# Kernel tuning notes

Measured on AMD Instinct MI355X. Metric: run time of the kernel, lower is better.

Reference implementation:

```python
import jax, jax.numpy as jnp
import numpy as np

N_NODES = 50000
N_EDGES = 800000
IN_CH = 256
OUT_CH = 64
HEADS = 4
NEG_SLOPE = 0.2


def setup_inputs() -> dict:
    key = jax.random.key(0)
    k = jax.random.split(key, 7)
    x = jax.random.normal(k[0], (N_NODES, IN_CH), dtype=jnp.float32)
    edge_index = jax.random.randint(k[1], (2, N_EDGES), 0, N_NODES, dtype=jnp.int32)
    # Glorot-style init for the linear projection and attention vectors
    W = jax.random.normal(k[2], (IN_CH, HEADS * OUT_CH), dtype=jnp.float32) / np.sqrt(IN_CH)
    att_src = jax.random.normal(k[3], (HEADS, OUT_CH), dtype=jnp.float32) / np.sqrt(OUT_CH)
    att_dst = jax.random.normal(k[4], (HEADS, OUT_CH), dtype=jnp.float32) / np.sqrt(OUT_CH)
    bias = jnp.zeros((HEADS * OUT_CH,), dtype=jnp.float32)
    return {"x": x, "edge_index": edge_index, "W": W,
            "att_src": att_src, "att_dst": att_dst, "bias": bias}


def reference(x, edge_index, W, att_src, att_dst, bias):
    N = x.shape[0]
    # PyG GATConv default: add self-loops
    loop = jnp.arange(N, dtype=edge_index.dtype)
    src = jnp.concatenate([edge_index[0], loop])
    dst = jnp.concatenate([edge_index[1], loop])

    h = (x @ W).reshape(N, HEADS, OUT_CH)          # [N,H,C]
    a_src = jnp.einsum('nhc,hc->nh', h, att_src)    # [N,H]
    a_dst = jnp.einsum('nhc,hc->nh', h, att_dst)    # [N,H]

    alpha = a_src[src] + a_dst[dst]                 # [E,H]
    alpha = jax.nn.leaky_relu(alpha, NEG_SLOPE)

    # segment softmax over edges grouped by destination node
    amax = jax.ops.segment_max(alpha, dst, num_segments=N)
    amax = jnp.where(jnp.isfinite(amax), amax, 0.0)
    e = jnp.exp(alpha - amax[dst])
    denom = jax.ops.segment_sum(e, dst, num_segments=N)
    coef = e / (denom[dst] + 1e-16)                 # [E,H]

    msg = coef[..., None] * h[src]                  # [E,H,C]
    out = jax.ops.segment_sum(msg, dst, num_segments=N)  # [N,H,C]
    out = out.reshape(N, HEADS * OUT_CH) + bias
    return jax.nn.relu(out)
```

## Files before the change

### kernel.cpp

```cpp
#include <hip/hip_runtime.h>
#include <hip/hip_bf16.h>

#define HC 256
#define NEG_SLOPE 0.2f
#define BM 64
#define BK 64
#define LDK 72

typedef short short8_t __attribute__((ext_vector_type(8)));
typedef float float4_t __attribute__((ext_vector_type(4)));
typedef int   int4_t   __attribute__((ext_vector_type(4)));

__device__ __forceinline__ unsigned short f2bf(float f) {
  unsigned u = __float_as_uint(f);
  return (unsigned short)((u + 0x7fffu + ((u >> 16) & 1u)) >> 16);
}
__device__ __forceinline__ float bf2f(unsigned short b) {
  return __uint_as_float(((unsigned)b) << 16);
}

__global__ void wt_kernel(const float* __restrict__ W, unsigned short* __restrict__ Wt)
{
  const int k = blockIdx.x;
  const int n = threadIdx.x;
  Wt[n * 256 + k] = f2bf(W[k * 256 + n]);
}

__global__ __launch_bounds__(256) void gemm_mfma(
    const float* __restrict__ x, const unsigned short* __restrict__ Wt,
    const float* __restrict__ att_src, const float* __restrict__ att_dst,
    unsigned short* __restrict__ h, float* __restrict__ a_src,
    float* __restrict__ a_dst, int nnodes)
{
  __shared__ unsigned short As[BM * LDK];
  __shared__ unsigned short Bs[256 * LDK];
  const int t    = threadIdx.x;
  const int wv   = t >> 6;
  const int lane = t & 63;
  const int r0   = blockIdx.x * BM;

  float4_t acc[4][4] = {};

  for (int k0 = 0; k0 < 256; k0 += BK) {
    __syncthreads();
    {
      const int row = t >> 2, kc = (t & 3) * 16;
      const int gr = r0 + row;
      float4 xv[4];
      if (gr < nnodes) {
        const float4* p = (const float4*)(x + (size_t)gr * 256 + k0 + kc);
        xv[0] = p[0]; xv[1] = p[1]; xv[2] = p[2]; xv[3] = p[3];
      } else {
        xv[0] = xv[1] = xv[2] = xv[3] = make_float4(0.f, 0.f, 0.f, 0.f);
      }
      const float* f = (const float*)xv;
      unsigned pk[8];
      #pragma unroll
      for (int i = 0; i < 8; ++i) {
        __hip_bfloat162 b2 = __float22bfloat162_rn(make_float2(f[2 * i], f[2 * i + 1]));
        pk[i] = *(unsigned*)&b2;
      }
      uint4* d = (uint4*)&As[row * LDK + kc];
      d[0] = make_uint4(pk[0], pk[1], pk[2], pk[3]);
      d[1] = make_uint4(pk[4], pk[5], pk[6], pk[7]);
    }
    #pragma unroll
    for (int it = 0; it < 4; ++it) {
      const int n = it * 64 + (t >> 2);
      const int kc = (t & 3) * 16;
      const uint4* g = (const uint4*)(Wt + (size_t)n * 256 + k0 + kc);
      uint4 v0 = g[0], v1 = g[1];
      uint4* d = (uint4*)&Bs[n * LDK + kc];
      d[0] = v0; d[1] = v1;
    }
    __syncthreads();

    #pragma unroll
    for (int ks = 0; ks < 2; ++ks) {
      const int ko = ks * 32 + (lane >> 4) * 8;
      short8_t af[4], bfr[4];
      #pragma unroll
      for (int mt = 0; mt < 4; ++mt)
        af[mt] = *(const short8_t*)&As[(16 * mt + (lane & 15)) * LDK + ko];
      #pragma unroll
      for (int nt = 0; nt < 4; ++nt)
        bfr[nt] = *(const short8_t*)&Bs[(64 * wv + 16 * nt + (lane & 15)) * LDK + ko];
      #pragma unroll
      for (int mt = 0; mt < 4; ++mt)
        #pragma unroll
        for (int nt = 0; nt < 4; ++nt)
          acc[mt][nt] = __builtin_amdgcn_mfma_f32_16x16x32_bf16(
              af[mt], bfr[nt], acc[mt][nt], 0, 0, 0);
    }
  }

  const int q = lane >> 4, l15 = lane & 15;
  float atts[4], attd[4];
  #pragma unroll
  for (int nt = 0; nt < 4; ++nt) {
    atts[nt] = att_src[wv * 64 + 16 * nt + l15];
    attd[nt] = att_dst[wv * 64 + 16 * nt + l15];
  }

  #pragma unroll
  for (int mt = 0; mt < 4; ++mt) {
    #pragma unroll
    for (int reg = 0; reg < 4; ++reg) {
      const int row = r0 + 16 * mt + 4 * q + reg;
      const bool ok = row < nnodes;
      float ps = 0.f, pd = 0.f;
      #pragma unroll
      for (int nt = 0; nt < 4; ++nt) {
        const float v = acc[mt][nt][reg];
        if (ok) h[(size_t)row * 256 + 64 * wv + 16 * nt + l15] = f2bf(v);
        ps += v * atts[nt];
        pd += v * attd[nt];
      }
      #pragma unroll
      for (int off = 8; off; off >>= 1) {
        ps += __shfl_down(ps, off, 16);
        pd += __shfl_down(pd, off, 16);
      }
      if (ok && l15 == 0) {
        a_src[row * 4 + wv] = ps;
        a_dst[row * 4 + wv] = pd;
      }
    }
  }
}

__global__ void deg_count(const int* __restrict__ ei, int* __restrict__ deg, int E)
{
  const int e = blockIdx.x * blockDim.x + threadIdx.x;
  if (e >= E) return;
  atomicAdd(&deg[ei[E + e]], 1);
}

__global__ __launch_bounds__(256) void scan_p1(const int* __restrict__ deg,
                                               int* __restrict__ bsum, int n)
{
  __shared__ int ws[4];
  const int t = threadIdx.x, lane = t & 63, wv = t >> 6;
  const int base = blockIdx.x * 1024 + t * 4;
  int4 v = make_int4(0, 0, 0, 0);
  if (base + 3 < n) v = *(const int4*)&deg[base];
  else {
    if (base + 0 < n) v.x = deg[base + 0];
    if (base + 1 < n) v.y = deg[base + 1];
    if (base + 2 < n) v.z = deg[base + 2];
  }
  int s = (v.x + v.y) + (v.z + v.w);
  #pragma unroll
  for (int off = 32; off; off >>= 1) s += __shfl_down(s, off, 64);
  if (lane == 0) ws[wv] = s;
  __syncthreads();
  if (t == 0) bsum[blockIdx.x] = (ws[0] + ws[1]) + (ws[2] + ws[3]);
}

__global__ __launch_bounds__(1024) void scan_p2(const int* __restrict__ bsum,
                                                int* __restrict__ boff,
                                                int* __restrict__ rowptr,
                                                int nb, int n)
{
  __shared__ int wsum[16], woff[16];
  const int t = threadIdx.x, lane = t & 63, wv = t >> 6;
  int v = (t < nb) ? bsum[t] : 0;
  int sc = v;
  #pragma unroll
  for (int off = 1; off < 64; off <<= 1) {
    int u = __shfl_up(sc, off, 64);
    if (lane >= off) sc += u;
  }
  if (lane == 63) wsum[wv] = sc;
  __syncthreads();
  if (t == 0) {
    int run = 0;
    #pragma unroll
    for (int i = 0; i < 16; ++i) { int x = wsum[i]; woff[i] = run; run += x; }
    rowptr[n] = run;
  }
  __syncthreads();
  if (t < nb) boff[t] = woff[wv] + sc - v;
}

__global__ __launch_bounds__(256) void scan_p3(const int* __restrict__ deg,
                                               const int* __restrict__ boff,
                                               int* __restrict__ rowptr,
                                               int* __restrict__ cursor, int n)
{
  __shared__ int wsum[4], woff[4];
  const int t = threadIdx.x, lane = t & 63, wv = t >> 6;
  const int base = blockIdx.x * 1024 + t * 4;
  int4 v = make_int4(0, 0, 0, 0);
  if (base + 3 < n) v = *(const int4*)&deg[base];
  else {
    if (base + 0 < n) v.x = deg[base + 0];
    if (base + 1 < n) v.y = deg[base + 1];
    if (base + 2 < n) v.z = deg[base + 2];
  }
  const int s = (v.x + v.y) + (v.z + v.w);
  int sc = s;
  #pragma unroll
  for (int off = 1; off < 64; off <<= 1) {
    int u = __shfl_up(sc, off, 64);
    if (lane >= off) sc += u;
  }
  if (lane == 63) wsum[wv] = sc;
  __syncthreads();
  if (t == 0) {
    int run = 0;
    #pragma unroll
    for (int i = 0; i < 4; ++i) { int x = wsum[i]; woff[i] = run; run += x; }
  }
  __syncthreads();
  int excl = boff[blockIdx.x] + woff[wv] + (sc - s);
  int4 r;
  r.x = excl;
  r.y = r.x + v.x;
  r.z = r.y + v.y;
  r.w = r.z + v.z;
  if (base + 3 < n) {
    *(int4*)&rowptr[base] = r;
    *(int4*)&cursor[base] = r;
  } else {
    if (base + 0 < n) { rowptr[base + 0] = r.x; cursor[base + 0] = r.x; }
    if (base + 1 < n) { rowptr[base + 1] = r.y; cursor[base + 1] = r.y; }
    if (base + 2 < n) { rowptr[base + 2] = r.z; cursor[base + 2] = r.z; }
  }
}

__global__ __launch_bounds__(256) void fill_csr(
    const int* __restrict__ ei, int* __restrict__ cursor,
    int* __restrict__ csr_src, int E, int nnodes)
{
  const int g    = blockIdx.x & 7;
  const int bg   = blockIdx.x >> 3;
  const int nbg  = gridDim.x >> 3;
  const int gsz  = (nnodes + 7) >> 3;
  const int dlo  = g * gsz;
  const int dhi  = min(dlo + gsz, nnodes);

  for (int e = bg * 256 + threadIdx.x; e < E; e += nbg * 256) {
    const int d = ei[E + e];
    if (d < dlo || d >= dhi) continue;
    const int pos = atomicAdd(&cursor[d], 1);
    csr_src[pos] = ei[e];
  }
}

__device__ __forceinline__ float4 ld_h(const unsigned short* __restrict__ h,
                                       int row, int cb)
{
  const ushort4 u = *(const ushort4*)&h[(size_t)row * 256 + cb];
  return make_float4(bf2f(u.x), bf2f(u.y), bf2f(u.z), bf2f(u.w));
}

__device__ __forceinline__ float edge_w(float as, float ad)
{
  float al = as + ad;
  al = al > 0.f ? al : NEG_SLOPE * al;
  return expf(al);
}

__global__ __launch_bounds__(256) void gather_kernel(
    const int* __restrict__ rowptr, const int* __restrict__ csr_src,
    const unsigned short* __restrict__ h,
    const float* __restrict__ a_src, const float* __restrict__ a_dst,
    const float* __restrict__ bias, float* __restrict__ out, int n)
{
  const int wave = threadIdx.x >> 6;
  const int lane = threadIdx.x & 63;
  const int d = blockIdx.x * 4 + wave;
  if (d >= n) return;

  const int head = lane >> 4;
  const int cb   = lane * 4;

  const float ad = a_dst[d * 4 + head];

  const float w = edge_w(a_src[d * 4 + head], ad);
  float dsum = w;
  float4 hv = ld_h(h, d, cb);
  float4 acc = make_float4(w * hv.x, w * hv.y, w * hv.z, w * hv.w);

  int j = rowptr[d];
  const int end = rowptr[d + 1];

  int4_t sC = {0, 0, 0, 0};
  if (j + 3 < end)
    sC = __builtin_nontemporal_load((const int4_t*)&csr_src[j]);
  while (j + 3 < end) {
    const int jn = j + 4;
    const int jp = (jn + 3 < end) ? jn : j;
    const int4_t sN = __builtin_nontemporal_load((const int4_t*)&csr_src[jp]);

    const float as0 = a_src[sC.x * 4 + head];
    const float as1 = a_src[sC.y * 4 + head];
    const float as2 = a_src[sC.z * 4 + head];
    const float as3 = a_src[sC.w * 4 + head];
    const float4 h0 = ld_h(h, sC.x, cb);
    const float4 h1 = ld_h(h, sC.y, cb);
    const float4 h2 = ld_h(h, sC.z, cb);
    const float4 h3 = ld_h(h, sC.w, cb);

    const float w0 = edge_w(as0, ad);
    const float w1 = edge_w(as1, ad);
    const float w2 = edge_w(as2, ad);
    const float w3 = edge_w(as3, ad);

    dsum += (w0 + w1) + (w2 + w3);
    acc.x += w0 * h0.x + w1 * h1.x + w2 * h2.x + w3 * h3.x;
    acc.y += w0 * h0.y + w1 * h1.y + w2 * h2.y + w3 * h3.y;
    acc.z += w0 * h0.z + w1 * h1.z + w2 * h2.z + w3 * h3.z;
    acc.w += w0 * h0.w + w1 * h1.w + w2 * h2.w + w3 * h3.w;

    sC = sN; j = jn;
  }
  for (; j < end; ++j) {
    const int s0 = csr_src[j];
    const float w0 = edge_w(a_src[s0 * 4 + head], ad);
    const float4 h0 = ld_h(h, s0, cb);
    dsum += w0;
    acc.x += w0 * h0.x; acc.y += w0 * h0.y;
    acc.z += w0 * h0.z; acc.w += w0 * h0.w;
  }

  const float inv = 1.f / (dsum + 1e-16f);
  const float4 b4 = ((const float4*)bias)[lane];
  float4 o;
  o.x = acc.x * inv + b4.x; o.x = o.x > 0.f ? o.x : 0.f;
  o.y = acc.y * inv + b4.y; o.y = o.y > 0.f ? o.y : 0.f;
  o.z = acc.z * inv + b4.z; o.z = o.z > 0.f ? o.z : 0.f;
  o.w = acc.w * inv + b4.w; o.w = o.w > 0.f ? o.w : 0.f;
  *(float4*)&out[(size_t)d * 256 + cb] = o;
}

extern "C" void kernel_launch(void* const* d_in, const int* in_sizes, int n_in,
                              void* d_out, int out_size, void* d_ws, size_t ws_size,
                              hipStream_t stream)
{
  const float* x       = (const float*)d_in[0];
  const int*   ei      = (const int*)d_in[1];
  const float* W       = (const float*)d_in[2];
  const float* att_src = (const float*)d_in[3];
  const float* att_dst = (const float*)d_in[4];
  const float* bias    = (const float*)d_in[5];

  const int nnodes = in_sizes[0] / HC;
  const int E      = in_sizes[1] / 2;
  const int nb     = (nnodes + 1023) / 1024;

  float* out = (float*)d_out;
  char* ws = (char*)d_ws;
  unsigned short* h  = (unsigned short*)ws;
  float* a_src = (float*)(ws + (size_t)nnodes * HC * 2);
  float* a_dst = a_src + (size_t)nnodes * 4;
  unsigned short* Wt = (unsigned short*)(a_dst + (size_t)nnodes * 4);
  int* deg    = (int*)((char*)Wt + 256 * 256 * 2);
  int* rowptr = deg + nnodes;
  int* cursor = rowptr + ((nnodes + 1 + 3) & ~3);
  int* bsum   = cursor + nnodes;
  int* boff   = bsum + ((nb + 3) & ~3);
  int* csr    = boff + ((nb + 3) & ~3);

  hipMemsetAsync(deg, 0, (size_t)nnodes * sizeof(int), stream);

  wt_kernel<<<256, 256, 0, stream>>>(W, Wt);

  gemm_mfma<<<(nnodes + BM - 1) / BM, 256, 0, stream>>>(
      x, Wt, att_src, att_dst, h, a_src, a_dst, nnodes);

  deg_count<<<(E + 255) / 256, 256, 0, stream>>>(ei, deg, E);
  scan_p1<<<nb, 256, 0, stream>>>(deg, bsum, nnodes);
  scan_p2<<<1, 1024, 0, stream>>>(bsum, boff, rowptr, nb, nnodes);
  scan_p3<<<nb, 256, 0, stream>>>(deg, boff, rowptr, cursor, nnodes);

  fill_csr<<<1024, 256, 0, stream>>>(ei, cursor, csr, E, nnodes);

  gather_kernel<<<(nnodes + 3) / 4, 256, 0, stream>>>(
      rowptr, csr, h, a_src, a_dst, bias, out, nnodes);
}
```

Baseline: 275.0 us.

## Fuse CSR build and weight transpose into one cooperative kernel

Replaces the memset, weight-transpose, degree count, three scan kernels and CSR fill with a single cooperative launch that separates the phases with grid-wide syncs. The aim is to remove several kernel launch gaps and the tail latency of small kernels. It requires all 1024 blocks to be co-resident, and the block-sum scan is cut to a single wavefront, which assumes at most 64 scan blocks.

After: 769.3 us. 180% more time.

```diff
diff --git a/kernel.cpp b/kernel.cpp
--- a/kernel.cpp
+++ b/kernel.cpp
@@ -1,5 +1,8 @@
 #include <hip/hip_runtime.h>
 #include <hip/hip_bf16.h>
+#include <hip/hip_cooperative_groups.h>
+
+namespace cg = cooperative_groups;
 
 #define HC 256
 #define NEG_SLOPE 0.2f
@@ -19,11 +22,116 @@
   return __uint_as_float(((unsigned)b) << 16);
 }
 
-__global__ void wt_kernel(const float* __restrict__ W, unsigned short* __restrict__ Wt)
-{
-  const int k = blockIdx.x;
-  const int n = threadIdx.x;
-  Wt[n * 256 + k] = f2bf(W[k * 256 + n]);
+__global__ __launch_bounds__(256) void csr_coop(
+    const float* __restrict__ W, unsigned short* __restrict__ Wt,
+    const int* __restrict__ ei, int* __restrict__ deg,
+    int* __restrict__ rowptr, int* __restrict__ cursor,
+    int* __restrict__ bsum, int* __restrict__ boff,
+    int* __restrict__ csr_src, int E, int n)
+{
+  cg::grid_group grid = cg::this_grid();
+  const int t   = threadIdx.x;
+  const int bid = blockIdx.x;
+  const int nbk = gridDim.x;
+  const int lane = t & 63, wv = t >> 6;
+  __shared__ int ws[4];
+  __shared__ int wsum[4], woff[4];
+
+  for (int i = bid * 256 + t; i < n; i += nbk * 256) deg[i] = 0;
+  if (bid < 256) Wt[t * 256 + bid] = f2bf(W[bid * 256 + t]);
+  grid.sync();
+
+  for (int e = bid * 256 + t; e < E; e += nbk * 256)
+    atomicAdd(&deg[ei[E + e]], 1);
+  grid.sync();
+
+  const int nb = (n + 1023) / 1024;
+  if (bid < nb) {
+    const int base = bid * 1024 + t * 4;
+    int4 v = make_int4(0, 0, 0, 0);
+    if (base + 3 < n) v = *(const int4*)&deg[base];
+    else {
+      if (base + 0 < n) v.x = deg[base + 0];
+      if (base + 1 < n) v.y = deg[base + 1];
+      if (base + 2 < n) v.z = deg[base + 2];
+    }
+    int s = (v.x + v.y) + (v.z + v.w);
+    #pragma unroll
+    for (int off = 32; off; off >>= 1) s += __shfl_down(s, off, 64);
+    if (lane == 0) ws[wv] = s;
+    __syncthreads();
+    if (t == 0) bsum[bid] = (ws[0] + ws[1]) + (ws[2] + ws[3]);
+  }
+  grid.sync();
+
+  if (bid == 0 && t < 64) {
+    const int v = (t < nb) ? bsum[t] : 0;
+    int sc = v;
+    #pragma unroll
+    for (int off = 1; off < 64; off <<= 1) {
+      int u = __shfl_up(sc, off, 64);
+      if (t >= off) sc += u;
+    }
+    if (t < nb) boff[t] = sc - v;
+    if (t == 63) rowptr[n] = sc;
+  }
+  grid.sync();
+
+  if (bid < nb) {
+    const int base = bid * 1024 + t * 4;
+    int4 v = make_int4(0, 0, 0, 0);
+    if (base + 3 < n) v = *(const int4*)&deg[base];
+    else {
+      if (base + 0 < n) v.x = deg[base + 0];
+      if (base + 1 < n) v.y = deg[base + 1];
+      if (base + 2 < n) v.z = deg[base + 2];
+    }
+    const int s = (v.x + v.y) + (v.z + v.w);
+    int sc = s;
+    #pragma unroll
+    for (int off = 1; off < 64; off <<= 1) {
+      int u = __shfl_up(sc, off, 64);
+      if (lane >= off) sc += u;
+    }
+    if (lane == 63) wsum[wv] = sc;
+    __syncthreads();
+    if (t == 0) {
+      int run = 0;
+      #pragma unroll
+      for (int i = 0; i < 4; ++i) { int x = wsum[i]; woff[i] = run; run += x; }
+    }
+    __syncthreads();
+    const int excl = boff[bid] + woff[wv] + (sc - s);
+    int4 r;
+    r.x = excl;
+    r.y = r.x + v.x;
+    r.z = r.y + v.y;
+    r.w = r.z + v.z;
+    if (base + 3 < n) {
+      *(int4*)&rowptr[base] = r;
+      *(int4*)&cursor[base] = r;
+    } else {
+      if (base + 0 < n) { rowptr[base + 0] = r.x; cursor[base + 0] = r.x; }
+      if (base + 1 < n) { rowptr[base + 1] = r.y; cursor[base + 1] = r.y; }
+      if (base + 2 < n) { rowptr[base + 2] = r.z; cursor[base + 2] = r.z; }
+    }
+  }
+  grid.sync();
+
+  {
+    const int g    = bid & 7;
+    const int bg   = bid >> 3;
+    const int nbg  = nbk >> 3;
+    const int gsz  = (n + 7) >> 3;
+    const int dlo  = g * gsz;
+    const int dhi  = min(dlo + gsz, n);
+    for (int e = bg * 256 + t; e < E; e += nbg * 256) {
+      const int d = ei[E + e];
+      if (d < dlo || d >= dhi) continue;
+      const int pos = atomicAdd(&cursor[d], 1);
+      csr_src[pos] = ei[e];
+    }
+  }
 }
 
 __global__ __launch_bounds__(256) void gemm_mfma(
@@ -126,125 +234,6 @@
         a_dst[row * 4 + wv] = pd;
       }
     }
-  }
-}
-
-__global__ void deg_count(const int* __restrict__ ei, int* __restrict__ deg, int E)
-{
-  const int e = blockIdx.x * blockDim.x + threadIdx.x;
-  if (e >= E) return;
-  atomicAdd(&deg[ei[E + e]], 1);
-}
-
-__global__ __launch_bounds__(256) void scan_p1(const int* __restrict__ deg,
-                                               int* __restrict__ bsum, int n)
-{
-  __shared__ int ws[4];
-  const int t = threadIdx.x, lane = t & 63, wv = t >> 6;
-  const int base = blockIdx.x * 1024 + t * 4;
-  int4 v = make_int4(0, 0, 0, 0);
-  if (base + 3 < n) v = *(const int4*)&deg[base];
-  else {
-    if (base + 0 < n) v.x = deg[base + 0];
-    if (base + 1 < n) v.y = deg[base + 1];
-    if (base + 2 < n) v.z = deg[base + 2];
-  }
-  int s = (v.x + v.y) + (v.z + v.w);
-  #pragma unroll
-  for (int off = 32; off; off >>= 1) s += __shfl_down(s, off, 64);
-  if (lane == 0) ws[wv] = s;
-  __syncthreads();
-  if (t == 0) bsum[blockIdx.x] = (ws[0] + ws[1]) + (ws[2] + ws[3]);
-}
-
-__global__ __launch_bounds__(1024) void scan_p2(const int* __restrict__ bsum,
-                                                int* __restrict__ boff,
-                                                int* __restrict__ rowptr,
-                                                int nb, int n)
-{
-  __shared__ int wsum[16], woff[16];
-  const int t = threadIdx.x, lane = t & 63, wv = t >> 6;
-  int v = (t < nb) ? bsum[t] : 0;
-  int sc = v;
-  #pragma unroll
-  for (int off = 1; off < 64; off <<= 1) {
-    int u = __shfl_up(sc, off, 64);
-    if (lane >= off) sc += u;
-  }
-  if (lane == 63) wsum[wv] = sc;
-  __syncthreads();
-  if (t == 0) {
-    int run = 0;
-    #pragma unroll
-    for (int i = 0; i < 16; ++i) { int x = wsum[i]; woff[i] = run; run += x; }
-    rowptr[n] = run;
-  }
-  __syncthreads();
-  if (t < nb) boff[t] = woff[wv] + sc - v;
-}
-
-__global__ __launch_bounds__(256) void scan_p3(const int* __restrict__ deg,
-                                               const int* __restrict__ boff,
-                                               int* __restrict__ rowptr,
-                                               int* __restrict__ cursor, int n)
-{
-  __shared__ int wsum[4], woff[4];
-  const int t = threadIdx.x, lane = t & 63, wv = t >> 6;
-  const int base = blockIdx.x * 1024 + t * 4;
-  int4 v = make_int4(0, 0, 0, 0);
-  if (base + 3 < n) v = *(const int4*)&deg[base];
-  else {
-    if (base + 0 < n) v.x = deg[base + 0];
-    if (base + 1 < n) v.y = deg[base + 1];
-    if (base + 2 < n) v.z = deg[base + 2];
-  }
-  const int s = (v.x + v.y) + (v.z + v.w);
-  int sc = s;
-  #pragma unroll
-  for (int off = 1; off < 64; off <<= 1) {
-    int u = __shfl_up(sc, off, 64);
-    if (lane >= off) sc += u;
-  }
-  if (lane == 63) wsum[wv] = sc;
-  __syncthreads();
-  if (t == 0) {
-    int run = 0;
-    #pragma unroll
-    for (int i = 0; i < 4; ++i) { int x = wsum[i]; woff[i] = run; run += x; }
-  }
-  __syncthreads();
-  int excl = boff[blockIdx.x] + woff[wv] + (sc - s);
-  int4 r;
-  r.x = excl;
-  r.y = r.x + v.x;
-  r.z = r.y + v.y;
-  r.w = r.z + v.z;
-  if (base + 3 < n) {
-    *(int4*)&rowptr[base] = r;
-    *(int4*)&cursor[base] = r;
-  } else {
-    if (base + 0 < n) { rowptr[base + 0] = r.x; cursor[base + 0] = r.x; }
-    if (base + 1 < n) { rowptr[base + 1] = r.y; cursor[base + 1] = r.y; }
-    if (base + 2 < n) { rowptr[base + 2] = r.z; cursor[base + 2] = r.z; }
-  }
-}
-
-__global__ __launch_bounds__(256) void fill_csr(
-    const int* __restrict__ ei, int* __restrict__ cursor,
-    int* __restrict__ csr_src, int E, int nnodes)
-{
-  const int g    = blockIdx.x & 7;
-  const int bg   = blockIdx.x >> 3;
-  const int nbg  = gridDim.x >> 3;
-  const int gsz  = (nnodes + 7) >> 3;
-  const int dlo  = g * gsz;
-  const int dhi  = min(dlo + gsz, nnodes);
-
-  for (int e = bg * 256 + threadIdx.x; e < E; e += nbg * 256) {
-    const int d = ei[E + e];
-    if (d < dlo || d >= dhi) continue;
-    const int pos = atomicAdd(&cursor[d], 1);
-    csr_src[pos] = ei[e];
   }
 }
 
@@ -363,20 +352,19 @@
   int* boff   = bsum + ((nb + 3) & ~3);
   int* csr    = boff + ((nb + 3) & ~3);
 
-  hipMemsetAsync(deg, 0, (size_t)nnodes * sizeof(int), stream);
-
-  wt_kernel<<<256, 256, 0, stream>>>(W, Wt);
+  {
+    void* args[] = {
+      (void*)&W, (void*)&Wt, (void*)&ei, (void*)&deg,
+      (void*)&rowptr, (void*)&cursor, (void*)&bsum, (void*)&boff,
+      (void*)&csr, (void*)&E, (void*)&nnodes
+    };
+    hipLaunchCooperativeKernel((void*)csr_coop, dim3(1024), dim3(256),
+                               args, 0, stream);
+  }
 
   gemm_mfma<<<(nnodes + BM - 1) / BM, 256, 0, stream>>>(
       x, Wt, att_src, att_dst, h, a_src, a_dst, nnodes);
 
-  deg_count<<<(E + 255) / 256, 256, 0, stream>>>(ei, deg, E);
-  scan_p1<<<nb, 256, 0, stream>>>(deg, bsum, nnodes);
-  scan_p2<<<1, 1024, 0, stream>>>(bsum, boff, rowptr, nb, nnodes);
-  scan_p3<<<nb, 256, 0, stream>>>(deg, boff, rowptr, cursor, nnodes);
-
-  fill_csr<<<1024, 256, 0, stream>>>(ei, cursor, csr, E, nnodes);
-
   gather_kernel<<<(nnodes + 3) / 4, 256, 0, stream>>>(
       rowptr, csr, h, a_src, a_dst, bias, out, nnodes);
 }
```

## Stage full A tile once in GEMM, read W directly, fold deg memset

Applied to the files above, without the earlier changes.

The GEMM kernel now converts and stores the whole 64x256 bf16 slice of x into shared memory in one pass, with a single barrier. The B operand (transposed bf16 W) is read straight from global memory through the caches instead of being staged through a second LDS buffer. This removes the per-K-step barriers and the repeated LDS fill of W, and lowers LDS use per block. Separately, zeroing of the degree array moves into wt_kernel, dropping the separate memset call. That fused zeroing only covers up to 65536 nodes, and the direct global B loads lean on cache hit rates.

Measured after the change: 279.9 us. Within noise of the previous version (+1.8%).

```diff
diff --git a/kernel.cpp b/kernel.cpp
--- a/kernel.cpp
+++ b/kernel.cpp
@@ -4,8 +4,7 @@
 #define HC 256
 #define NEG_SLOPE 0.2f
 #define BM 64
-#define BK 64
-#define LDK 72
+#define LDKF 264
 
 typedef short short8_t __attribute__((ext_vector_type(8)));
 typedef float float4_t __attribute__((ext_vector_type(4)));
@@ -19,11 +18,14 @@
   return __uint_as_float(((unsigned)b) << 16);
 }
 
-__global__ void wt_kernel(const float* __restrict__ W, unsigned short* __restrict__ Wt)
+__global__ void wt_kernel(const float* __restrict__ W, unsigned short* __restrict__ Wt,
+                          int* __restrict__ deg, int n)
 {
   const int k = blockIdx.x;
-  const int n = threadIdx.x;
-  Wt[n * 256 + k] = f2bf(W[k * 256 + n]);
+  const int t = threadIdx.x;
+  Wt[t * 256 + k] = f2bf(W[k * 256 + t]);
+  const int i = k * 256 + t;
+  if (i < n) deg[i] = 0;
 }
 
 __global__ __launch_bounds__(256) void gemm_mfma(
@@ -32,23 +34,20 @@
     unsigned short* __restrict__ h, float* __restrict__ a_src,
     float* __restrict__ a_dst, int nnodes)
 {
-  __shared__ unsigned short As[BM * LDK];
-  __shared__ unsigned short Bs[256 * LDK];
+  __shared__ unsigned short As[BM * LDKF];
   const int t    = threadIdx.x;
   const int wv   = t >> 6;
   const int lane = t & 63;
   const int r0   = blockIdx.x * BM;
 
-  float4_t acc[4][4] = {};
-
-  for (int k0 = 0; k0 < 256; k0 += BK) {
-    __syncthreads();
-    {
-      const int row = t >> 2, kc = (t & 3) * 16;
-      const int gr = r0 + row;
+  {
+    const int row = t >> 2, kcb = (t & 3) * 16;
+    const int gr = r0 + row;
+    #pragma unroll
+    for (int k0 = 0; k0 < 256; k0 += 64) {
       float4 xv[4];
       if (gr < nnodes) {
-        const float4* p = (const float4*)(x + (size_t)gr * 256 + k0 + kc);
+        const float4* p = (const float4*)(x + (size_t)gr * 256 + k0 + kcb);
         xv[0] = p[0]; xv[1] = p[1]; xv[2] = p[2]; xv[3] = p[3];
       } else {
         xv[0] = xv[1] = xv[2] = xv[3] = make_float4(0.f, 0.f, 0.f, 0.f);
@@ -60,41 +59,36 @@
         __hip_bfloat162 b2 = __float22bfloat162_rn(make_float2(f[2 * i], f[2 * i + 1]));
         pk[i] = *(unsigned*)&b2;
       }
-      uint4* d = (uint4*)&As[row * LDK + kc];
+      uint4* d = (uint4*)&As[row * LDKF + k0 + kcb];
       d[0] = make_uint4(pk[0], pk[1], pk[2], pk[3]);
       d[1] = make_uint4(pk[4], pk[5], pk[6], pk[7]);
     }
-    #pragma unroll
-    for (int it = 0; it < 4; ++it) {
-      const int n = it * 64 + (t >> 2);
-      const int kc = (t & 3) * 16;
-      const uint4* g = (const uint4*)(Wt + (size_t)n * 256 + k0 + kc);
-      uint4 v0 = g[0], v1 = g[1];
-      uint4* d = (uint4*)&Bs[n * LDK + kc];
-      d[0] = v0; d[1] = v1;
-    }
-    __syncthreads();
-
-    #pragma unroll
-    for (int ks = 0; ks < 2; ++ks) {
-      const int ko = ks * 32 + (lane >> 4) * 8;
-      short8_t af[4], bfr[4];
-      #pragma unroll
-      for (int mt = 0; mt < 4; ++mt)
-        af[mt] = *(const short8_t*)&As[(16 * mt + (lane & 15)) * LDK + ko];
+  }
+  __syncthreads();
+
+  const int l15 = lane & 15, q = lane >> 4;
+  float4_t acc[4][4] = {};
+
+  const unsigned short* __restrict__ Bp = Wt + ((size_t)(64 * wv + l15)) * 256 + q * 8;
+
+  #pragma unroll
+  for (int kstep = 0; kstep < 8; ++kstep) {
+    const int ko = kstep * 32;
+    short8_t bfr[4], af[4];
+    #pragma unroll
+    for (int nt = 0; nt < 4; ++nt)
+      bfr[nt] = *(const short8_t*)(Bp + nt * 16 * 256 + ko);
+    #pragma unroll
+    for (int mt = 0; mt < 4; ++mt)
+      af[mt] = *(const short8_t*)&As[(16 * mt + l15) * LDKF + ko + q * 8];
+    #pragma unroll
+    for (int mt = 0; mt < 4; ++mt)
       #pragma unroll
       for (int nt = 0; nt < 4; ++nt)
-        bfr[nt] = *(const short8_t*)&Bs[(64 * wv + 16 * nt + (lane & 15)) * LDK + ko];
-      #pragma unroll
-      for (int mt = 0; mt < 4; ++mt)
-        #pragma unroll
-        for (int nt = 0; nt < 4; ++nt)
-          acc[mt][nt] = __builtin_amdgcn_mfma_f32_16x16x32_bf16(
-              af[mt], bfr[nt], acc[mt][nt], 0, 0, 0);
-    }
-  }
-
-  const int q = lane >> 4, l15 = lane & 15;
+        acc[mt][nt] = __builtin_amdgcn_mfma_f32_16x16x32_bf16(
+            af[mt], bfr[nt], acc[mt][nt], 0, 0, 0);
+  }
+
   float atts[4], attd[4];
   #pragma unroll
   for (int nt = 0; nt < 4; ++nt) {
@@ -363,9 +357,7 @@
   int* boff   = bsum + ((nb + 3) & ~3);
   int* csr    = boff + ((nb + 3) & ~3);
 
-  hipMemsetAsync(deg, 0, (size_t)nnodes * sizeof(int), stream);
-
-  wt_kernel<<<256, 256, 0, stream>>>(W, Wt);
+  wt_kernel<<<256, 256, 0, stream>>>(W, Wt, deg, nnodes);
 
   gemm_mfma<<<(nnodes + BM - 1) / BM, 256, 0, stream>>>(
       x, Wt, att_src, att_dst, h, a_src, a_dst, nnodes);
```
